# Kernel optimization log

Hardware: AMD Instinct MI355X
Metric: run time of the kernel (lower is better)

## Reference

```python
import jax, jax.numpy as jnp
import numpy as np
from jax import lax


def leaky(x):
    return jax.nn.leaky_relu(x, 0.01)


def masked_softmax(vec, mask, eps=1e-6):
    # softmax over entries where mask>0; zero elsewhere (stable via masked max)
    mask = mask.astype(vec.dtype)
    mx = jnp.max(jnp.where(mask > 0, vec, -jnp.inf), axis=1, keepdims=True)
    mx = jnp.where(jnp.isfinite(mx), mx, 0.0)
    e = jnp.exp(vec - mx) * mask
    return e / (e.sum(axis=1, keepdims=True) + eps)


def gru_dir(x, w_ih, w_hh, b_ih, b_hh, reverse):
    # PyTorch GRU cell math, one direction. x: [T, in]
    gi_all = x @ w_ih.T + b_ih  # [T, 3*GH], input gates precomputed
    def step(h, gi):
        gh = h @ w_hh.T + b_hh
        i_r, i_z, i_n = jnp.split(gi, 3)
        h_r, h_z, h_n = jnp.split(gh, 3)
        r = jax.nn.sigmoid(i_r + h_r)
        z = jax.nn.sigmoid(i_z + h_z)
        n = jnp.tanh(i_n + r * h_n)
        h2 = (1.0 - z) * n + z * h
        return h2, h2
    h0 = jnp.zeros((w_hh.shape[1],), x.dtype)
    _, ys = lax.scan(step, h0, gi_all, reverse=reverse)
    return ys  # [T, GH]


def setup_inputs():
    key = jax.random.key(0)
    ks = jax.random.split(key, 30)
    W, P, R, H = 128, 4096, 8192, 1024
    GH = H // 2
    s = 0.05
    def nrm(k, shp, sc):
        return jax.random.normal(k, shp, jnp.float32) * sc
    return {
        "word_feat": nrm(ks[0], (W, H), 1.0),
        "phrase_feat": nrm(ks[1], (P, H), 1.0),
        "rel_feat": nrm(ks[2], (R, H), 1.0),
        "w_ih_f": nrm(ks[3], (3 * GH, H), s), "w_hh_f": nrm(ks[4], (3 * GH, GH), s),
        "b_ih_f": nrm(ks[5], (3 * GH,), s), "b_hh_f": nrm(ks[6], (3 * GH,), s),
        "w_ih_b": nrm(ks[7], (3 * GH, H), s), "w_hh_b": nrm(ks[8], (3 * GH, GH), s),
        "b_ih_b": nrm(ks[9], (3 * GH,), s), "b_hh_b": nrm(ks[10], (3 * GH,), s),
        "w2p_w_W": nrm(ks[11], (H, H), s), "w2p_w_b": nrm(ks[12], (H,), s),
        "w2p_p_W": nrm(ks[13], (H, H), s), "w2p_p_b": nrm(ks[14], (H,), s),
        "w2p_t_W": nrm(ks[15], (H, H), s), "w2p_t_b": nrm(ks[16], (H,), s),
        "rel_W": nrm(ks[17], (H, 3 * H), s), "rel_b": nrm(ks[18], (H,), s),
        "att1_W": nrm(ks[19], (H, 4 * H), s), "att1_b": nrm(ks[20], (H,), s),
        "att2_W": nrm(ks[21], (1, H), s), "att2_b": nrm(ks[22], (1,), s),
        "r2p_t_W": nrm(ks[23], (H, H), s), "r2p_t_b": nrm(ks[24], (H,), s),
        "rel_conn_mat": jax.random.randint(ks[25], (2, R), 0, P),
        "word_to_graph_conn": jax.random.randint(ks[26], (P, W), 0, 2),
    }


def reference(word_feat, phrase_feat, rel_feat, w_ih_f, w_hh_f, b_ih_f, b_hh_f,
              w_ih_b, w_hh_b, b_ih_b, b_hh_b, w2p_w_W, w2p_w_b, w2p_p_W, w2p_p_b,
              w2p_t_W, w2p_t_b, rel_W, rel_b, att1_W, att1_b, att2_W, att2_b,
              r2p_t_W, r2p_t_b, rel_conn_mat, word_to_graph_conn):
    H = word_feat.shape[1]
    # bidirectional GRU over the word sequence
    lf = jnp.concatenate([
        gru_dir(word_feat, w_ih_f, w_hh_f, b_ih_f, b_hh_f, False),
        gru_dir(word_feat, w_ih_b, w_hh_b, b_ih_b, b_hh_b, True),
    ], axis=1)  # [T, H]
    ctx = jnp.concatenate([lf[0], lf[-1]])[None, :]  # [1, 2H]
    # word -> phrase attention
    a = (leaky(phrase_feat @ w2p_p_W.T + w2p_p_b)
         @ leaky(word_feat @ w2p_w_W.T + w2p_w_b).T) / jnp.sqrt(jnp.float32(H))
    a = masked_softmax(a, word_to_graph_conn)
    upd = phrase_feat + (a @ word_feat) @ w2p_t_W.T + w2p_t_b  # [P, H]
    # phrase -> rel
    sub, obj = rel_conn_mat[0], rel_conn_mat[1]
    Rn = sub.shape[0]
    Pn = upd.shape[0]
    urel = jnp.concatenate([upd[sub], upd[obj], rel_feat], 1) @ rel_W.T + rel_b  # [R, H]
    # rel -> phrase with sparse connectivity (each rel touches subject+object)
    ar = jnp.arange(Rn)
    mask = jnp.zeros((Pn, Rn), upd.dtype).at[sub, ar].set(1.0).at[obj, ar].set(1.0)
    ix = jnp.concatenate([sub, obj])
    iy = jnp.concatenate([ar, ar])
    fuse = jnp.concatenate(
        [upd[ix], urel[iy], jnp.broadcast_to(ctx, (ix.shape[0], ctx.shape[1]))], 1)  # [2R, 4H]
    s = (leaky(fuse @ att1_W.T + att1_b) @ att2_W.T + att2_b)[:, 0]
    att = jnp.zeros((Pn, Rn), upd.dtype).at[ix, iy].set(s)
    att = masked_softmax(att, mask)
    out_phrase = upd + (att @ urel) @ r2p_t_W.T + r2p_t_b
    return (word_feat, out_phrase, urel)
```

## Files before the change

kernel.cpp:

```cpp
#include <hip/hip_runtime.h>

#define DEV __device__ __forceinline__

typedef short s16x8 __attribute__((ext_vector_type(8)));
typedef float f32x4 __attribute__((ext_vector_type(4)));
typedef __fp16 fp16x8 __attribute__((ext_vector_type(8)));
typedef unsigned short u16;
typedef unsigned long long u64;

constexpr int Wn = 128;
constexpr int Pn = 4096;
constexpr int Rn = 8192;
constexpr int Hn = 1024;

DEV float b2f(u16 u) { union { unsigned i; float f; } x; x.i = (unsigned)u << 16; return x.f; }
DEV u16 f2b(float f) {
  union { float f; unsigned i; } x; x.f = f;
  unsigned r = x.i + 0x7FFF + ((x.i >> 16) & 1);
  return (u16)(r >> 16);
}
DEV u16 f2h(float x) { __fp16 h = (__fp16)x; u16 r; __builtin_memcpy(&r, &h, 2); return r; }
DEV float leaky(float x) { return x >= 0.f ? x : 0.01f * x; }

DEV void load_lds16(const void* g, void* l) {
  __builtin_amdgcn_global_load_lds(
      (const __attribute__((address_space(1))) void*)g,
      (__attribute__((address_space(3))) void*)l, 16, 0, 0);
}

DEV float wred_sum(float v) {
  #pragma unroll
  for (int m = 1; m < 64; m <<= 1) v += __shfl_xor(v, m, 64);
  return v;
}
DEV float wred_max(float v) {
  #pragma unroll
  for (int m = 1; m < 64; m <<= 1) v = fmaxf(v, __shfl_xor(v, m, 64));
  return v;
}

template<bool OUTF32, bool ACT, bool BIAS, bool RES, bool DUAL>
DEV void gemm_tile(char* sm,
    const u16* __restrict__ A, int lda, const u16* __restrict__ B, int ldb,
    void* Cp, int ldc, const float* __restrict__ bias,
    const float* res, int ldr, u16* C16, float alpha, int K, int m0, int n0)
{
  char* As = sm;
  char* Bs = sm + 16384;
  const int tid = threadIdx.x;
  const int lane = tid & 63, w = tid >> 6;
  const int wr = (w >> 1) * 64, wc = (w & 1) * 64;
  const int r_lo = lane & 15, kq = lane >> 4;

  __syncthreads();

  f32x4 acc[4][4];
  #pragma unroll
  for (int i = 0; i < 4; ++i)
    #pragma unroll
    for (int j = 0; j < 4; ++j) acc[i][j] = (f32x4){0.f, 0.f, 0.f, 0.f};

  for (int kt = 0; kt < K; kt += 64) {
    if (kt) __syncthreads();
    #pragma unroll
    for (int i = 0; i < 4; ++i) {
      int f = i * 4096 + tid * 16;
      int row = f >> 7, colb = f & 127;
      int scol = colb ^ ((row & 7) << 4);
      load_lds16((const char*)(A + (size_t)(m0 + row) * lda + kt) + scol,
                 As + i * 4096 + w * 1024);
    }
    #pragma unroll
    for (int i = 0; i < 4; ++i) {
      int f = i * 4096 + tid * 16;
      int row = f >> 7, colb = f & 127;
      int scol = colb ^ ((row & 7) << 4);
      load_lds16((const char*)(B + (size_t)(n0 + row) * ldb + kt) + scol,
                 Bs + i * 4096 + w * 1024);
    }
    __syncthreads();
    #pragma unroll
    for (int ks = 0; ks < 2; ++ks) {
      s16x8 af[4], bfr[4];
      const int kb = ks * 64 + kq * 16;
      #pragma unroll
      for (int mi = 0; mi < 4; ++mi) {
        int row = wr + mi * 16 + r_lo;
        af[mi] = *(const s16x8*)(As + row * 128 + (kb ^ ((row & 7) << 4)));
      }
      #pragma unroll
      for (int ni = 0; ni < 4; ++ni) {
        int row = wc + ni * 16 + r_lo;
        bfr[ni] = *(const s16x8*)(Bs + row * 128 + (kb ^ ((row & 7) << 4)));
      }
      #pragma unroll
      for (int mi = 0; mi < 4; ++mi)
        #pragma unroll
        for (int ni = 0; ni < 4; ++ni)
          acc[mi][ni] = __builtin_amdgcn_mfma_f32_16x16x32_bf16(af[mi], bfr[ni], acc[mi][ni], 0, 0, 0);
    }
  }
  #pragma unroll
  for (int mi = 0; mi < 4; ++mi)
    #pragma unroll
    for (int ni = 0; ni < 4; ++ni)
      #pragma unroll
      for (int j = 0; j < 4; ++j) {
        int r = m0 + wr + mi * 16 + kq * 4 + j;
        int c = n0 + wc + ni * 16 + r_lo;
        float v = acc[mi][ni][j] * alpha;
        if (BIAS) v += bias[c];
        if (RES)  v += res[(size_t)r * ldr + c];
        if (ACT)  v = leaky(v);
        if (OUTF32) ((float*)Cp)[(size_t)r * ldc + c] = v;
        else        ((u16*)Cp)[(size_t)r * ldc + c] = f2b(v);
        if (DUAL)   C16[(size_t)r * ldc + c] = f2b(v);
      }
}

template<bool OUTF32, bool ACT, bool BIAS, bool RES, bool DUAL>
__global__ __launch_bounds__(256) void k_gemm_bt(
    const u16* __restrict__ A, int lda, const u16* __restrict__ B, int ldb,
    void* Cp, int ldc, const float* __restrict__ bias,
    const float* res, int ldr, u16* C16, float alpha, int K)
{
  __shared__ __align__(16) char sm[32768];
  gemm_tile<OUTF32, ACT, BIAS, RES, DUAL>(sm, A, lda, B, ldb, Cp, ldc, bias,
      res, ldr, C16, alpha, K, blockIdx.y * 128, blockIdx.x * 128);
}

DEV void gemm_tile_bf32(char* sm,
    const u16* __restrict__ A, int lda, const float* __restrict__ Bf, int ldb,
    float* __restrict__ C, int ldc, const float* __restrict__ bias,
    int K, int m0, int n0)
{
  char* As = sm;
  char* Bs = sm + 16384;
  const int tid = threadIdx.x;
  const int lane = tid & 63, w = tid >> 6;
  const int wr = (w >> 1) * 64, wc = (w & 1) * 64;
  const int r_lo = lane & 15, kq = lane >> 4;

  __syncthreads();

  f32x4 acc[4][4];
  #pragma unroll
  for (int i = 0; i < 4; ++i)
    #pragma unroll
    for (int j = 0; j < 4; ++j) acc[i][j] = (f32x4){0.f, 0.f, 0.f, 0.f};

  for (int kt = 0; kt < K; kt += 64) {
    if (kt) __syncthreads();
    #pragma unroll
    for (int i = 0; i < 4; ++i) {
      int f = i * 4096 + tid * 16;
      int row = f >> 7, colb = f & 127;
      int scol = colb ^ ((row & 7) << 4);
      load_lds16((const char*)(A + (size_t)(m0 + row) * lda + kt) + scol,
                 As + i * 4096 + w * 1024);
    }
    #pragma unroll
    for (int i = 0; i < 4; ++i) {
      int e = i * 2048 + tid * 8;
      int row = e >> 6, col = e & 63;
      const float* s = Bf + (size_t)(n0 + row) * ldb + kt + col;
      float4 a4 = *(const float4*)s;
      float4 b4 = *(const float4*)(s + 4);
      u16 d8[8] = {f2b(a4.x), f2b(a4.y), f2b(a4.z), f2b(a4.w),
                   f2b(b4.x), f2b(b4.y), f2b(b4.z), f2b(b4.w)};
      int byte = (col * 2) ^ ((row & 7) << 4);
      *(uint4*)(Bs + row * 128 + byte) = *(uint4*)d8;
    }
    __syncthreads();
    #pragma unroll
    for (int ks = 0; ks < 2; ++ks) {
      s16x8 af[4], bfr[4];
      const int kb = ks * 64 + kq * 16;
      #pragma unroll
      for (int mi = 0; mi < 4; ++mi) {
        int row = wr + mi * 16 + r_lo;
        af[mi] = *(const s16x8*)(As + row * 128 + (kb ^ ((row & 7) << 4)));
      }
      #pragma unroll
      for (int ni = 0; ni < 4; ++ni) {
        int row = wc + ni * 16 + r_lo;
        bfr[ni] = *(const s16x8*)(Bs + row * 128 + (kb ^ ((row & 7) << 4)));
      }
      #pragma unroll
      for (int mi = 0; mi < 4; ++mi)
        #pragma unroll
        for (int ni = 0; ni < 4; ++ni)
          acc[mi][ni] = __builtin_amdgcn_mfma_f32_16x16x32_bf16(af[mi], bfr[ni], acc[mi][ni], 0, 0, 0);
    }
  }
  #pragma unroll
  for (int mi = 0; mi < 4; ++mi)
    #pragma unroll
    for (int ni = 0; ni < 4; ++ni)
      #pragma unroll
      for (int j = 0; j < 4; ++j) {
        int r = m0 + wr + mi * 16 + kq * 4 + j;
        int c = n0 + wc + ni * 16 + r_lo;
        C[(size_t)r * ldc + c] = acc[mi][ni][j] + bias[c];
      }
}

__global__ __launch_bounds__(256) void k_gemm_af32(
    const float* __restrict__ A, int lda, const u16* __restrict__ B, int ldb,
    u16* __restrict__ C, int ldc, int K)
{
  __shared__ __align__(16) char sm[32768];
  char* As = sm;
  char* Bs = sm + 16384;
  const int tid = threadIdx.x;
  const int lane = tid & 63, w = tid >> 6;
  const int m0 = blockIdx.y * 128, n0 = blockIdx.x * 128;
  const int wr = (w >> 1) * 64, wc = (w & 1) * 64;
  const int r_lo = lane & 15, kq = lane >> 4;

  f32x4 acc[4][4];
  #pragma unroll
  for (int i = 0; i < 4; ++i)
    #pragma unroll
    for (int j = 0; j < 4; ++j) acc[i][j] = (f32x4){0.f, 0.f, 0.f, 0.f};

  for (int kt = 0; kt < K; kt += 64) {
    if (kt) __syncthreads();
    #pragma unroll
    for (int i = 0; i < 4; ++i) {
      int e = i * 2048 + tid * 8;
      int row = e >> 6, col = e & 63;
      const float* s = A + (size_t)(m0 + row) * lda + kt + col;
      float4 a4 = *(const float4*)s;
      float4 b4 = *(const float4*)(s + 4);
      u16 d8[8] = {f2b(a4.x), f2b(a4.y), f2b(a4.z), f2b(a4.w),
                   f2b(b4.x), f2b(b4.y), f2b(b4.z), f2b(b4.w)};
      int byte = (col * 2) ^ ((row & 7) << 4);
      *(uint4*)(As + row * 128 + byte) = *(uint4*)d8;
    }
    #pragma unroll
    for (int i = 0; i < 4; ++i) {
      int f = i * 4096 + tid * 16;
      int row = f >> 7, colb = f & 127;
      int scol = colb ^ ((row & 7) << 4);
      load_lds16((const char*)(B + (size_t)(n0 + row) * ldb + kt) + scol,
                 Bs + i * 4096 + w * 1024);
    }
    __syncthreads();
    #pragma unroll
    for (int ks = 0; ks < 2; ++ks) {
      s16x8 af[4], bfr[4];
      const int kb = ks * 64 + kq * 16;
      #pragma unroll
      for (int mi = 0; mi < 4; ++mi) {
        int row = wr + mi * 16 + r_lo;
        af[mi] = *(const s16x8*)(As + row * 128 + (kb ^ ((row & 7) << 4)));
      }
      #pragma unroll
      for (int ni = 0; ni < 4; ++ni) {
        int row = wc + ni * 16 + r_lo;
        bfr[ni] = *(const s16x8*)(Bs + row * 128 + (kb ^ ((row & 7) << 4)));
      }
      #pragma unroll
      for (int mi = 0; mi < 4; ++mi)
        #pragma unroll
        for (int ni = 0; ni < 4; ++ni)
          acc[mi][ni] = __builtin_amdgcn_mfma_f32_16x16x32_bf16(af[mi], bfr[ni], acc[mi][ni], 0, 0, 0);
    }
  }
  #pragma unroll
  for (int mi = 0; mi < 4; ++mi)
    #pragma unroll
    for (int ni = 0; ni < 4; ++ni)
      #pragma unroll
      for (int j = 0; j < 4; ++j) {
        int r = m0 + wr + mi * 16 + kq * 4 + j;
        int c = n0 + wc + ni * 16 + r_lo;
        C[(size_t)r * ldc + c] = f2b(acc[mi][ni][j]);
      }
}

__global__ __launch_bounds__(256) void k_rf3(
    const u16* __restrict__ G, const u16* __restrict__ relU,
    const u16* __restrict__ W3s, const float* __restrict__ rel_b,
    float* __restrict__ out_urel)
{
  __shared__ __align__(16) char sm[32768];
  int half = blockIdx.y >> 5;
  gemm_tile<true, false, true, false, false>(sm,
      half ? relU : G, Hn, W3s, Hn,
      out_urel + (size_t)half * 4096 * Hn, Hn, rel_b, nullptr, 0, nullptr,
      1.f, Hn, (blockIdx.y & 31) * 128, blockIdx.x * 128);
}

__global__ __launch_bounds__(256) void k_gemm_rel(
    const u16* __restrict__ upd16, const int* __restrict__ rcm,
    const u16* __restrict__ W1, const u16* __restrict__ W2,
    float* __restrict__ out_urel)
{
  __shared__ __align__(16) char sm[32768];
  __shared__ int ridx[2][128];
  char* As = sm;
  char* Bs = sm + 16384;
  const int tid = threadIdx.x;
  const int lane = tid & 63, w = tid >> 6;
  const int hh = blockIdx.y >> 5;
  const int m0 = (blockIdx.y & 31) * 128, n0 = blockIdx.x * 128;
  const int wr = (w >> 1) * 64, wc = (w & 1) * 64;
  const int r_lo = lane & 15, kq = lane >> 4;
  const int* sub = rcm + hh * 4096;
  const int* obj = rcm + Rn + hh * 4096;
  float* C = out_urel + (size_t)hh * 4096 * Hn;

  if (tid < 128) ridx[0][tid] = sub[m0 + tid];
  else ridx[1][tid - 128] = obj[m0 + tid - 128];
  __syncthreads();

  f32x4 acc[4][4];
  #pragma unroll
  for (int i = 0; i < 4; ++i)
    #pragma unroll
    for (int j = 0; j < 4; ++j) acc[i][j] = (f32x4){0.f, 0.f, 0.f, 0.f};

  for (int kt = 0; kt < 2048; kt += 64) {
    const int half = kt >> 10;
    const int kk = kt & 1023;
    const u16* Wm = half ? W2 : W1;
    __syncthreads();
    #pragma unroll
    for (int i = 0; i < 4; ++i) {
      int f = i * 4096 + tid * 16;
      int row = f >> 7, colb = f & 127;
      int scol = colb ^ ((row & 7) << 4);
      load_lds16((const char*)(upd16 + (size_t)ridx[half][row] * 1024 + kk) + scol,
                 As + i * 4096 + w * 1024);
    }
    #pragma unroll
    for (int i = 0; i < 4; ++i) {
      int f = i * 4096 + tid * 16;
      int row = f >> 7, colb = f & 127;
      int scol = colb ^ ((row & 7) << 4);
      load_lds16((const char*)(Wm + (size_t)(n0 + row) * 1024 + kk) + scol,
                 Bs + i * 4096 + w * 1024);
    }
    __syncthreads();
    #pragma unroll
    for (int ks = 0; ks < 2; ++ks) {
      s16x8 af[4], bfr[4];
      const int kb = ks * 64 + kq * 16;
      #pragma unroll
      for (int mi = 0; mi < 4; ++mi) {
        int row = wr + mi * 16 + r_lo;
        af[mi] = *(const s16x8*)(As + row * 128 + (kb ^ ((row & 7) << 4)));
      }
      #pragma unroll
      for (int ni = 0; ni < 4; ++ni) {
        int row = wc + ni * 16 + r_lo;
        bfr[ni] = *(const s16x8*)(Bs + row * 128 + (kb ^ ((row & 7) << 4)));
      }
      #pragma unroll
      for (int mi = 0; mi < 4; ++mi)
        #pragma unroll
        for (int ni = 0; ni < 4; ++ni)
          acc[mi][ni] = __builtin_amdgcn_mfma_f32_16x16x32_bf16(af[mi], bfr[ni], acc[mi][ni], 0, 0, 0);
    }
  }
  #pragma unroll
  for (int mi = 0; mi < 4; ++mi)
    #pragma unroll
    for (int ni = 0; ni < 4; ++ni)
      #pragma unroll
      for (int j = 0; j < 4; ++j) {
        int r = m0 + wr + mi * 16 + kq * 4 + j;
        int c = n0 + wc + ni * 16 + r_lo;
        C[(size_t)r * Hn + c] = acc[mi][ni][j] + C[(size_t)r * Hn + c];
      }
}

struct CvtTask { const float* src; u16* dst; int sld; int units; };
struct MKArgs {
  const float *w_hh_f, *w_hh_b, *b_hh_f, *b_hh_b;
  const float *word_feat, *w_ih_f, *w_ih_b, *b_ih_f, *b_ih_b;
  const float *w2p_w_b, *w2p_p_b;
  const int *rcm, *conn;
  float *gi_f, *gi_b, *scores, *ctx;
  u16 *wf16, *wl, *pf16, *w2pw16, *w2pp16, *pl, *attw, *wfT, *aw;
  u64* X; int* pc; int* cnt2; int* offs; int* cursor;
  CvtTask t[12]; int nt;
};

__global__ __launch_bounds__(256) void k_mega(MKArgs a)
{
  __shared__ __align__(16) u16 wlds[96 * 512];
  __shared__ float bh[96];
  __shared__ float partg[4][96];
  __shared__ __align__(16) u16 hb[512];

  const int bid = blockIdx.x;
  const int tid = threadIdx.x;
  const int lane = tid & 63, wv = tid >> 6;
  const int NW = (int)gridDim.x - 32;

  if (bid >= 32) {
    const int bc = bid - 32, nb = NW;
    int bar = 0;
    auto wbarrier = [&]() {
      __syncthreads();
      if (tid == 0) {
        __hip_atomic_fetch_add(&a.pc[bar], 1, __ATOMIC_ACQ_REL, __HIP_MEMORY_SCOPE_AGENT);
        while (__hip_atomic_load(&a.pc[bar], __ATOMIC_ACQUIRE, __HIP_MEMORY_SCOPE_AGENT) < NW)
          __builtin_amdgcn_s_sleep(4);
      }
      __syncthreads();
      ++bar;
    };
    auto cvt_task = [&](const float* src, int sld, u16* dst, int units) {
      for (int u = bc * 256 + tid; u < units; u += nb * 256) {
        int row = u >> 7, c = (u & 127) * 8;
        const float* s = src + (size_t)row * sld + c;
        float4 va = *(const float4*)s;
        float4 vb = *(const float4*)(s + 4);
        ushort4 lo = {f2b(va.x), f2b(va.y), f2b(va.z), f2b(va.w)};
        ushort4 hi = {f2b(vb.x), f2b(vb.y), f2b(vb.z), f2b(vb.w)};
        *(ushort4*)(dst + (size_t)row * 1024 + c) = lo;
        *(ushort4*)(dst + (size_t)row * 1024 + c + 4) = hi;
      }
    };

    cvt_task(a.word_feat, Hn, a.wf16, Wn * 128);
    wbarrier();
    if (bc < 24) {
      const float* Bm = bc < 12 ? a.w_ih_f : a.w_ih_b;
      float* Cm = bc < 12 ? a.gi_f : a.gi_b;
      const float* bm = bc < 12 ? a.b_ih_f : a.b_ih_b;
      gemm_tile_bf32((char*)wlds, a.wf16, Hn, Bm, Hn, Cm, 1536, bm, Hn,
                     0, (bc % 12) * 128);
      __syncthreads();
      if (tid == 0)
        __hip_atomic_fetch_add(&a.pc[32], 1, __ATOMIC_ACQ_REL, __HIP_MEMORY_SCOPE_AGENT);
    }
    for (int u = bc * 256 + tid; u < 2 * Rn; u += nb * 256) {
      if (u < Rn && a.rcm[u] == a.rcm[Rn + u]) continue;
      atomicAdd(a.cnt2 + a.rcm[u], 1);
    }
    for (int k = 0; k < a.nt; ++k)
      cvt_task(a.t[k].src, a.t[k].sld, a.t[k].dst, a.t[k].units);
    wbarrier();
    if (bc == 0) {
      int* part = (int*)wlds;
      int* pscan = part + 256;
      int loc[16]; int s = 0;
      #pragma unroll
      for (int i = 0; i < 16; ++i) { loc[i] = a.cnt2[tid * 16 + i]; s += loc[i]; }
      part[tid] = s; __syncthreads();
      if (tid == 0) { int acc = 0; for (int i = 0; i < 256; ++i) { pscan[i] = acc; acc += part[i]; } }
      __syncthreads();
      int base = pscan[tid];
      #pragma unroll
      for (int i = 0; i < 16; ++i) {
        a.offs[tid * 16 + i] = base; a.cursor[tid * 16 + i] = base; base += loc[i];
      }
      if (tid == 255) a.offs[Pn] = base;
      __syncthreads();
    }
    for (int u = bc; u < 264; u += nb) {
      if (u < 8)
        gemm_tile<false, true, true, false, false>((char*)wlds, a.wf16, Hn,
            a.w2pw16, Hn, a.wl, Hn, a.w2p_w_b, nullptr, 0, nullptr, 1.f, Hn,
            0, u * 128);
      else {
        int t2 = u - 8;
        gemm_tile<false, true, true, false, false>((char*)wlds, a.pf16, Hn,
            a.w2pp16, Hn, a.pl, Hn, a.w2p_p_b, nullptr, 0, nullptr, 1.f, Hn,
            (t2 >> 3) * 128, (t2 & 7) * 128);
      }
    }
    wbarrier();
    for (int u = bc; u < 544; u += nb) {
      if (u < 32)
        gemm_tile<true, false, false, false, false>((char*)wlds, a.pl, Hn,
            a.wl, Hn, a.scores, Wn, nullptr, nullptr, 0, nullptr, 0.03125f, Hn,
            u * 128, 0);
      else {
        int idx = (u - 32) * 256 + tid;
        int r = idx >> 10, c = idx & 1023;
        a.wfT[c * 128 + r] = a.wf16[idx];
      }
    }
    wbarrier();
    for (int u = bc; u < 1024; u += nb) {
      int p = u * 4 + wv;
      float v0 = a.scores[(size_t)p * 128 + lane];
      float v1 = a.scores[(size_t)p * 128 + 64 + lane];
      int m0 = a.conn[(size_t)p * 128 + lane];
      int m1 = a.conn[(size_t)p * 128 + 64 + lane];
      float x0 = m0 > 0 ? v0 : -INFINITY;
      float x1 = m1 > 0 ? v1 : -INFINITY;
      float mx = wred_max(fmaxf(x0, x1));
      if (!(mx > -INFINITY)) mx = 0.f;
      float e0 = m0 > 0 ? __expf(v0 - mx) : 0.f;
      float e1 = m1 > 0 ? __expf(v1 - mx) : 0.f;
      float s = wred_sum(e0 + e1);
      float inv = 1.f / (s + 1e-6f);
      a.attw[(size_t)p * 128 + lane] = f2b(e0 * inv);
      a.attw[(size_t)p * 128 + 64 + lane] = f2b(e1 * inv);
    }
    wbarrier();
    for (int u = bc; u < 256; u += nb)
      gemm_tile<false, false, false, false, false>((char*)wlds, a.attw, Wn,
          a.wfT, Wn, a.aw, Hn, nullptr, nullptr, 0, nullptr, 1.f, Wn,
          (u >> 3) * 128, (u & 7) * 128);
    return;
  }

  const int dir = bid >> 4;
  const int b   = bid & 15;
  const float* w_hh = dir ? a.w_hh_b : a.w_hh_f;
  const float* b_hhp = dir ? a.b_hh_b : a.b_hh_f;
  const float* gi = dir ? a.gi_b : a.gi_f;
  u64* Xd = a.X + (size_t)dir * 128 * 256;

  for (int idx = tid; idx < 96 * 128; idx += 256) {
    int gl = idx >> 7;
    int kc = (idx & 127) << 2;
    int g  = 32 * b + (gl & 31) + ((gl >> 5) << 9);
    float4 wv4 = *(const float4*)(w_hh + (size_t)g * 512 + kc);
    u16 d4[4] = {f2h(wv4.x), f2h(wv4.y), f2h(wv4.z), f2h(wv4.w)};
    int byte = (kc * 2) ^ ((gl & 7) << 4);
    *(uint2*)((char*)wlds + gl * 1024 + byte) = *(uint2*)d4;
  }
  if (tid < 96) {
    int g = 32 * b + (tid & 31) + ((tid >> 5) << 9);
    bh[tid] = b_hhp[g];
  }
  for (int i = tid; i < 256; i += 256) ((unsigned*)hb)[i] = 0u;
  if (tid == 0) {
    while (__hip_atomic_load(&a.pc[32], __ATOMIC_ACQUIRE, __HIP_MEMORY_SCOPE_AGENT) < 24)
      __builtin_amdgcn_s_sleep(8);
  }
  __syncthreads();

  float hprev = 0.f;
  const int jg = 32 * b + tid;
  const int r_lo = lane & 15, kq = lane >> 4;
  const fp16x8 zf = {0, 0, 0, 0, 0, 0, 0, 0};

  for (int sidx = 0; sidx < 128; ++sidx) {
    const int t = dir ? (127 - sidx) : sidx;

    float gir = 0.f, giz = 0.f, gin = 0.f;
    if (tid < 32) {
      gir = gi[t * 1536 + jg];
      giz = gi[t * 1536 + 512 + jg];
      gin = gi[t * 1536 + 1024 + jg];
    }

    f32x4 acc6[6];
    #pragma unroll
    for (int gt = 0; gt < 6; ++gt) acc6[gt] = (f32x4){0.f, 0.f, 0.f, 0.f};
    #pragma unroll
    for (int k2 = 0; k2 < 4; ++k2) {
      int kt = (wv << 2) + k2;
      fp16x8 bf = (r_lo == 0) ? *(const fp16x8*)(hb + kt * 32 + kq * 8) : zf;
      #pragma unroll
      for (int gt = 0; gt < 6; ++gt) {
        int gl = gt * 16 + r_lo;
        int byte = (kt * 64 + kq * 16) ^ ((gl & 7) << 4);
        fp16x8 af = *(const fp16x8*)((const char*)wlds + gl * 1024 + byte);
        acc6[gt] = __builtin_amdgcn_mfma_f32_16x16x32_f16(af, bf, acc6[gt], 0, 0, 0);
      }
    }
    if (r_lo == 0) {
      #pragma unroll
      for (int gt = 0; gt < 6; ++gt)
        #pragma unroll
        for (int j = 0; j < 4; ++j)
          partg[wv][gt * 16 + kq * 4 + j] = acc6[gt][j];
    }
    __syncthreads();

    if (wv == 0) {
      float h2v = 0.f;
      if (lane < 32) {
        int j = lane;
        float ghr = partg[0][j] + partg[1][j] + partg[2][j] + partg[3][j] + bh[j];
        float ghz = partg[0][j + 32] + partg[1][j + 32] + partg[2][j + 32] + partg[3][j + 32] + bh[j + 32];
        float ghn = partg[0][j + 64] + partg[1][j + 64] + partg[2][j + 64] + partg[3][j + 64] + bh[j + 64];
        float rr = 1.f / (1.f + __expf(-(gir + ghr)));
        float zz = 1.f / (1.f + __expf(-(giz + ghz)));
        float nn = tanhf(gin + rr * ghn);
        h2v = (1.f - zz) * nn + zz * hprev;
        hprev = h2v;
        if (sidx == 0)   a.ctx[(dir ? 1536 : 0)    + jg] = h2v;
        if (sidx == 127) a.ctx[(dir ? 512  : 1024) + jg] = h2v;
      }
      if (sidx < 127) {
        float q0 = __shfl(h2v, (lane & 15) * 2, 64);
        float q1 = __shfl(h2v, (lane & 15) * 2 + 1, 64);
        if (lane < 16) {
          u64 pk = (u64)f2h(q0) | ((u64)f2h(q1) << 16) |
                   ((u64)(unsigned)(sidx + 1) << 32);
          __hip_atomic_store(&Xd[(size_t)sidx * 256 + b * 16 + lane], pk,
                             __ATOMIC_RELAXED, __HIP_MEMORY_SCOPE_AGENT);
        }
        const u64* src = Xd + (size_t)sidx * 256;
        const unsigned want = (unsigned)(sidx + 1);
        const int base = lane * 4;
        u64 v[4];
        unsigned done = 0;
        while (done != 0xFu) {
          #pragma unroll
          for (int i = 0; i < 4; ++i)
            if (!(done & (1u << i)))
              v[i] = __hip_atomic_load(&src[base + i], __ATOMIC_RELAXED,
                                       __HIP_MEMORY_SCOPE_AGENT);
          #pragma unroll
          for (int i = 0; i < 4; ++i)
            if (!(done & (1u << i)) && (unsigned)(v[i] >> 32) == want)
              done |= 1u << i;
          if (done != 0xFu) __builtin_amdgcn_s_sleep(1);
        }
        #pragma unroll
        for (int i = 0; i < 4; ++i)
          ((unsigned*)hb)[base + i] = (unsigned)v[i];
      }
    }
    __syncthreads();
  }
}

__global__ __launch_bounds__(256) void k_cvec(const float* __restrict__ att1W,
    const float* __restrict__ att1b, const float* __restrict__ ctx, float* __restrict__ cvec)
{
  int i = blockIdx.x * 4 + (threadIdx.x >> 6);
  int lane = threadIdx.x & 63;
  const float* wrow = att1W + (size_t)i * 4096 + 2048 + lane * 32;
  const float* cp = ctx + lane * 32;
  float acc = 0.f;
  #pragma unroll
  for (int k = 0; k < 32; ++k) acc += wrow[k] * cp[k];
  acc = wred_sum(acc);
  if (lane == 0) cvec[i] = acc + att1b[i];
}

__global__ __launch_bounds__(256) void k_edge_s(const int* __restrict__ rcm,
    const u16* __restrict__ U1, const u16* __restrict__ V1, const float* __restrict__ cvec,
    const float* __restrict__ att2w, const float* __restrict__ att2b,
    float* __restrict__ sval)
{
  int idx = blockIdx.x * 4 + (threadIdx.x >> 6);
  int lane = threadIdx.x & 63;
  int rL = idx < Rn ? idx : idx - Rn;
  int p = rcm[idx];
  const u16* u = U1 + (size_t)p * Hn + lane * 16;
  const u16* v = V1 + (size_t)rL * Hn + lane * 16;
  const float* aw = att2w + lane * 16;
  const float* cv = cvec + lane * 16;
  float acc = 0.f;
  #pragma unroll
  for (int i = 0; i < 16; ++i) {
    float x = b2f(u[i]) + b2f(v[i]) + cv[i];
    acc += aw[i] * leaky(x);
  }
  acc = wred_sum(acc);
  if (lane == 0) sval[idx] = acc + att2b[0];
}

__global__ __launch_bounds__(256) void k_fill(const int* __restrict__ rcm,
    const float* __restrict__ sval, int* __restrict__ cursor,
    int* __restrict__ er, float* __restrict__ es)
{
  int e = blockIdx.x * 256 + threadIdx.x;
  if (e < Rn && rcm[e] == rcm[Rn + e]) return;
  int slot = atomicAdd(cursor + rcm[e], 1);
  er[slot] = e & (Rn - 1);
  es[slot] = sval[e];
}

__global__ __launch_bounds__(256) void k_att_apply(const int* __restrict__ offs,
    const int* __restrict__ er, const float* __restrict__ es,
    const float* __restrict__ urel, u16* __restrict__ pacc)
{
  int p = blockIdx.x;
  int tid = threadIdx.x;
  int beg = offs[p], end = offs[p + 1];
  float mx = -INFINITY;
  for (int i = beg; i < end; ++i) mx = fmaxf(mx, es[i]);
  float den = 1e-6f;
  for (int i = beg; i < end; ++i) den += __expf(es[i] - mx);
  float inv = 1.f / den;
  float a0 = 0.f, a1 = 0.f, a2 = 0.f, a3 = 0.f;
  int c0 = tid * 4;
  for (int i = beg; i < end; ++i) {
    float wgt = __expf(es[i] - mx) * inv;
    float4 q = *(const float4*)(urel + (size_t)er[i] * Hn + c0);
    a0 += wgt * q.x; a1 += wgt * q.y; a2 += wgt * q.z; a3 += wgt * q.w;
  }
  ushort4 ov; ov.x = f2b(a0); ov.y = f2b(a1); ov.z = f2b(a2); ov.w = f2b(a3);
  *(ushort4*)(pacc + (size_t)p * Hn + c0) = ov;
}

extern "C" void kernel_launch(void* const* d_in, const int* in_sizes, int n_in,
                              void* d_out, int out_size, void* d_ws, size_t ws_size,
                              hipStream_t stream)
{
  const float* word_feat   = (const float*)d_in[0];
  const float* phrase_feat = (const float*)d_in[1];
  const float* rel_feat    = (const float*)d_in[2];
  const float* w_ih_f = (const float*)d_in[3];
  const float* w_hh_f = (const float*)d_in[4];
  const float* b_ih_f = (const float*)d_in[5];
  const float* b_hh_f = (const float*)d_in[6];
  const float* w_ih_b = (const float*)d_in[7];
  const float* w_hh_b = (const float*)d_in[8];
  const float* b_ih_b = (const float*)d_in[9];
  const float* b_hh_b = (const float*)d_in[10];
  const float* w2p_w_W = (const float*)d_in[11];
  const float* w2p_w_b = (const float*)d_in[12];
  const float* w2p_p_W = (const float*)d_in[13];
  const float* w2p_p_b = (const float*)d_in[14];
  const float* w2p_t_W = (const float*)d_in[15];
  const float* w2p_t_b = (const float*)d_in[16];
  const float* rel_W   = (const float*)d_in[17];
  const float* rel_b   = (const float*)d_in[18];
  const float* att1_W  = (const float*)d_in[19];
  const float* att1_b  = (const float*)d_in[20];
  const float* att2_W  = (const float*)d_in[21];
  const float* att2_b  = (const float*)d_in[22];
  const float* r2p_t_W = (const float*)d_in[23];
  const float* r2p_t_b = (const float*)d_in[24];
  const int* rcm  = (const int*)d_in[25];
  const int* conn = (const int*)d_in[26];

  float* out_word = (float*)d_out;
  float* out_phr  = out_word + (size_t)Wn * Hn;
  float* out_urel = out_phr + (size_t)Pn * Hn;

  char* ws = (char*)d_ws;
  size_t off = 0;
  auto alloc = [&](size_t bytes) -> char* {
    char* pptr = ws + off; off += (bytes + 255) & ~(size_t)255; return pptr;
  };
  int*   cnt2   = (int*)alloc(Pn * 4);
  int*   pc     = (int*)alloc(64 * 4);
  u64*   X      = (u64*)alloc(2 * 128 * 256 * 8);
  size_t zlen   = (size_t)((char*)(X + 2 * 128 * 256) - (char*)cnt2);
  float* ctx    = (float*)alloc(2048 * 4);
  float* cvec   = (float*)alloc(1024 * 4);
  int*   cursor = (int*)alloc(Pn * 4);
  int*   offs   = (int*)alloc((Pn + 1) * 4);
  int*   er     = (int*)alloc(2 * Rn * 4);
  float* es     = (float*)alloc(2 * Rn * 4);
  float* sval   = (float*)alloc(2 * Rn * 4);
  float* gi_f   = (float*)alloc(128 * 1536 * 4);
  float* gi_b   = (float*)alloc(128 * 1536 * 4);
  u16*   wf16   = (u16*)alloc((size_t)Wn * Hn * 2);
  u16*   wl     = (u16*)alloc((size_t)Wn * Hn * 2);
  u16*   upd16  = (u16*)alloc((size_t)Pn * Hn * 2);
  char*  RA     = alloc(16777216);
  u16*   W1s    = (u16*)RA;
  u16*   W2s    = (u16*)(RA + 2097152);
  u16*   W3s    = (u16*)(RA + 4194304);
  u16*   G      = (u16*)(RA + 6291456);
  u16*   V1f    = (u16*)RA;
  u16*   A1p16  = (u16*)alloc(2097152);
  u16*   A1r16  = (u16*)alloc(2097152);
  u16*   U1     = (u16*)alloc((size_t)Pn * Hn * 2);
  u16*   relU16 = U1;
  u16*   r2pW16 = (u16*)alloc(2097152);
  u16*   pacc   = upd16;

  float* scores = (float*)out_phr;
  char* urlB = (char*)out_urel;
  u16*   pf16   = (u16*)urlB;
  u16*   w2pw16 = (u16*)(urlB + 8388608);
  u16*   w2pp16 = (u16*)(urlB + 10485760);
  u16*   w2pt16 = (u16*)(urlB + 12582912);
  u16*   pl     = (u16*)(urlB + 14680064);
  u16*   aw     = (u16*)(urlB + 23068672);
  u16*   attw   = (u16*)(urlB + 31457280);
  u16*   wfT    = (u16*)(urlB + 32505856);

  (void)hipMemsetAsync(cnt2, 0, zlen, stream);

  dim3 blk(256);

  MKArgs A;
  A.w_hh_f = w_hh_f; A.w_hh_b = w_hh_b; A.b_hh_f = b_hh_f; A.b_hh_b = b_hh_b;
  A.word_feat = word_feat; A.w_ih_f = w_ih_f; A.w_ih_b = w_ih_b;
  A.b_ih_f = b_ih_f; A.b_ih_b = b_ih_b;
  A.w2p_w_b = w2p_w_b; A.w2p_p_b = w2p_p_b;
  A.rcm = rcm; A.conn = conn;
  A.gi_f = gi_f; A.gi_b = gi_b; A.scores = scores; A.ctx = ctx;
  A.wf16 = wf16; A.wl = wl;
  A.pf16 = pf16; A.w2pw16 = w2pw16; A.w2pp16 = w2pp16;
  A.pl = pl; A.attw = attw; A.wfT = wfT; A.aw = aw;
  A.X = X; A.pc = pc; A.cnt2 = cnt2; A.offs = offs; A.cursor = cursor;
  A.t[0]  = {phrase_feat,    pf16,   Hn,     Pn * 128};
  A.t[1]  = {w2p_w_W,        w2pw16, Hn,     1024 * 128};
  A.t[2]  = {w2p_p_W,        w2pp16, Hn,     1024 * 128};
  A.t[3]  = {w2p_t_W,        w2pt16, Hn,     1024 * 128};
  A.t[4]  = {rel_W,          W1s,    3 * Hn, 1024 * 128};
  A.t[5]  = {rel_W + Hn,     W2s,    3 * Hn, 1024 * 128};
  A.t[6]  = {rel_W + 2 * Hn, W3s,    3 * Hn, 1024 * 128};
  A.t[7]  = {att1_W,         A1p16,  4 * Hn, 1024 * 128};
  A.t[8]  = {att1_W + Hn,    A1r16,  4 * Hn, 1024 * 128};
  A.t[9]  = {r2p_t_W,        r2pW16, Hn,     1024 * 128};
  A.t[10] = {rel_feat,       G,      Hn,     4096 * 128};
  A.t[11] = {rel_feat + (size_t)4096 * Hn, relU16, Hn, 4096 * 128};
  A.nt = 12;
  k_mega<<<256, blk, 0, stream>>>(A);
  k_cvec<<<256, blk, 0, stream>>>(att1_W, att1_b, ctx, cvec);

  k_gemm_bt<true, false, true, true, true><<<dim3(8, 32), blk, 0, stream>>>(
      aw, Hn, w2pt16, Hn, out_phr, Hn, w2p_t_b, phrase_feat, Hn, upd16, 1.f, Hn);

  k_rf3<<<dim3(8, 64), blk, 0, stream>>>(G, relU16, W3s, rel_b, out_urel);
  k_gemm_rel<<<dim3(8, 64), blk, 0, stream>>>(upd16, rcm, W1s, W2s, out_urel);

  k_gemm_bt<false, false, false, false, false><<<dim3(8, 32), blk, 0, stream>>>(
      upd16, Hn, A1p16, Hn, U1, Hn, nullptr, nullptr, 0, nullptr, 1.f, Hn);
  k_gemm_af32<<<dim3(8, 64), blk, 0, stream>>>(
      out_urel, Hn, A1r16, Hn, V1f, Hn, Hn);

  k_edge_s<<<(2 * Rn) / 4, blk, 0, stream>>>(rcm, U1, V1f, cvec, att2_W, att2_b, sval);
  k_fill<<<(2 * Rn) / 256, blk, 0, stream>>>(rcm, sval, cursor, er, es);
  k_att_apply<<<Pn, blk, 0, stream>>>(offs, er, es, out_urel, pacc);
  k_gemm_bt<true, false, true, true, false><<<dim3(8, 32), blk, 0, stream>>>(
      pacc, Hn, r2pW16, Hn, out_phr, Hn, r2p_t_b, out_phr, Hn, nullptr, 1.f, Hn);

  (void)hipMemcpyAsync(out_word, word_feat, (size_t)Wn * Hn * 4,
                       hipMemcpyDeviceToDevice, stream);
}
```

Before: 764.6 us.

## Hold GRU recurrent weights in registers, widen persistent mega-kernel, fuse w2p_t GEMM

The GRU blocks now keep their W_hh fp16 MFMA fragments in registers instead of a 96KB LDS tile. That lets shared memory shrink to 32KB and allows three blocks per CU under launch_bounds(256,3). The grid grows from 256 to 736 blocks, giving the worker phase many more blocks. The separate w2p_t GEMM launch is folded into the mega-kernel after an extra grid barrier. This raises register pressure and relies on all 736 blocks being co-resident for the spin barriers, so it risks spills or deadlock if occupancy falls short.

```diff
diff --git a/kernel.cpp b/kernel.cpp
--- a/kernel.cpp
+++ b/kernel.cpp
@@ -381,17 +381,17 @@
 struct MKArgs {
   const float *w_hh_f, *w_hh_b, *b_hh_f, *b_hh_b;
   const float *word_feat, *w_ih_f, *w_ih_b, *b_ih_f, *b_ih_b;
-  const float *w2p_w_b, *w2p_p_b;
+  const float *phrase_feat, *w2p_w_b, *w2p_p_b, *w2p_t_b;
   const int *rcm, *conn;
-  float *gi_f, *gi_b, *scores, *ctx;
-  u16 *wf16, *wl, *pf16, *w2pw16, *w2pp16, *pl, *attw, *wfT, *aw;
+  float *gi_f, *gi_b, *scores, *out_phr, *ctx;
+  u16 *wf16, *wl, *pf16, *w2pw16, *w2pp16, *w2pt16, *pl, *attw, *wfT, *aw, *upd16;
   u64* X; int* pc; int* cnt2; int* offs; int* cursor;
   CvtTask t[12]; int nt;
 };
 
-__global__ __launch_bounds__(256) void k_mega(MKArgs a)
-{
-  __shared__ __align__(16) u16 wlds[96 * 512];
+__global__ __launch_bounds__(256, 3) void k_mega(MKArgs a)
+{
+  __shared__ __align__(16) char sm[32768];
   __shared__ float bh[96];
   __shared__ float partg[4][96];
   __shared__ __align__(16) u16 hb[512];
@@ -433,7 +433,7 @@
       const float* Bm = bc < 12 ? a.w_ih_f : a.w_ih_b;
       float* Cm = bc < 12 ? a.gi_f : a.gi_b;
       const float* bm = bc < 12 ? a.b_ih_f : a.b_ih_b;
-      gemm_tile_bf32((char*)wlds, a.wf16, Hn, Bm, Hn, Cm, 1536, bm, Hn,
+      gemm_tile_bf32(sm, a.wf16, Hn, Bm, Hn, Cm, 1536, bm, Hn,
                      0, (bc % 12) * 128);
       __syncthreads();
       if (tid == 0)
@@ -447,7 +447,7 @@
       cvt_task(a.t[k].src, a.t[k].sld, a.t[k].dst, a.t[k].units);
     wbarrier();
     if (bc == 0) {
-      int* part = (int*)wlds;
+      int* part = (int*)sm;
       int* pscan = part + 256;
       int loc[16]; int s = 0;
       #pragma unroll
@@ -465,12 +465,12 @@
     }
     for (int u = bc; u < 264; u += nb) {
       if (u < 8)
-        gemm_tile<false, true, true, false, false>((char*)wlds, a.wf16, Hn,
+        gemm_tile<false, true, true, false, false>(sm, a.wf16, Hn,
             a.w2pw16, Hn, a.wl, Hn, a.w2p_w_b, nullptr, 0, nullptr, 1.f, Hn,
             0, u * 128);
       else {
         int t2 = u - 8;
-        gemm_tile<false, true, true, false, false>((char*)wlds, a.pf16, Hn,
+        gemm_tile<false, true, true, false, false>(sm, a.pf16, Hn,
             a.w2pp16, Hn, a.pl, Hn, a.w2p_p_b, nullptr, 0, nullptr, 1.f, Hn,
             (t2 >> 3) * 128, (t2 & 7) * 128);
       }
@@ -478,7 +478,7 @@
     wbarrier();
     for (int u = bc; u < 544; u += nb) {
       if (u < 32)
-        gemm_tile<true, false, false, false, false>((char*)wlds, a.pl, Hn,
+        gemm_tile<true, false, false, false, false>(sm, a.pl, Hn,
             a.wl, Hn, a.scores, Wn, nullptr, nullptr, 0, nullptr, 0.03125f, Hn,
             u * 128, 0);
       else {
@@ -507,9 +507,14 @@
     }
     wbarrier();
     for (int u = bc; u < 256; u += nb)
-      gemm_tile<false, false, false, false, false>((char*)wlds, a.attw, Wn,
+      gemm_tile<false, false, false, false, false>(sm, a.attw, Wn,
           a.wfT, Wn, a.aw, Hn, nullptr, nullptr, 0, nullptr, 1.f, Wn,
           (u >> 3) * 128, (u & 7) * 128);
+    wbarrier();
+    for (int u = bc; u < 256; u += nb)
+      gemm_tile<true, false, true, true, true>(sm, a.aw, Hn,
+          a.w2pt16, Hn, a.out_phr, Hn, a.w2p_t_b, a.phrase_feat, Hn, a.upd16,
+          1.f, Hn, (u >> 3) * 128, (u & 7) * 128);
     return;
   }
 
@@ -519,15 +524,27 @@
   const float* b_hhp = dir ? a.b_hh_b : a.b_hh_f;
   const float* gi = dir ? a.gi_b : a.gi_f;
   u64* Xd = a.X + (size_t)dir * 128 * 256;
-
-  for (int idx = tid; idx < 96 * 128; idx += 256) {
-    int gl = idx >> 7;
-    int kc = (idx & 127) << 2;
-    int g  = 32 * b + (gl & 31) + ((gl >> 5) << 9);
-    float4 wv4 = *(const float4*)(w_hh + (size_t)g * 512 + kc);
-    u16 d4[4] = {f2h(wv4.x), f2h(wv4.y), f2h(wv4.z), f2h(wv4.w)};
-    int byte = (kc * 2) ^ ((gl & 7) << 4);
-    *(uint2*)((char*)wlds + gl * 1024 + byte) = *(uint2*)d4;
+  const int r_lo = lane & 15, kq = lane >> 4;
+
+  fp16x8 wfrag[4][6];
+  #pragma unroll
+  for (int k2 = 0; k2 < 4; ++k2) {
+    int kt = (wv << 2) + k2;
+    int col = kt * 32 + kq * 8;
+    #pragma unroll
+    for (int gt = 0; gt < 6; ++gt) {
+      int gl = gt * 16 + r_lo;
+      int g = 32 * b + (gl & 31) + ((gl >> 5) << 9);
+      const float* s = w_hh + (size_t)g * 512 + col;
+      float4 lo4 = *(const float4*)s;
+      float4 hi4 = *(const float4*)(s + 4);
+      fp16x8 f;
+      f[0] = (__fp16)lo4.x; f[1] = (__fp16)lo4.y;
+      f[2] = (__fp16)lo4.z; f[3] = (__fp16)lo4.w;
+      f[4] = (__fp16)hi4.x; f[5] = (__fp16)hi4.y;
+      f[6] = (__fp16)hi4.z; f[7] = (__fp16)hi4.w;
+      wfrag[k2][gt] = f;
+    }
   }
   if (tid < 96) {
     int g = 32 * b + (tid & 31) + ((tid >> 5) << 9);
@@ -542,7 +559,6 @@
 
   float hprev = 0.f;
   const int jg = 32 * b + tid;
-  const int r_lo = lane & 15, kq = lane >> 4;
   const fp16x8 zf = {0, 0, 0, 0, 0, 0, 0, 0};
 
   for (int sidx = 0; sidx < 128; ++sidx) {
@@ -563,12 +579,8 @@
       int kt = (wv << 2) + k2;
       fp16x8 bf = (r_lo == 0) ? *(const fp16x8*)(hb + kt * 32 + kq * 8) : zf;
       #pragma unroll
-      for (int gt = 0; gt < 6; ++gt) {
-        int gl = gt * 16 + r_lo;
-        int byte = (kt * 64 + kq * 16) ^ ((gl & 7) << 4);
-        fp16x8 af = *(const fp16x8*)((const char*)wlds + gl * 1024 + byte);
-        acc6[gt] = __builtin_amdgcn_mfma_f32_16x16x32_f16(af, bf, acc6[gt], 0, 0, 0);
-      }
+      for (int gt = 0; gt < 6; ++gt)
+        acc6[gt] = __builtin_amdgcn_mfma_f32_16x16x32_f16(wfrag[k2][gt], bf, acc6[gt], 0, 0, 0);
     }
     if (r_lo == 0) {
       #pragma unroll
@@ -789,12 +801,12 @@
   A.w_hh_f = w_hh_f; A.w_hh_b = w_hh_b; A.b_hh_f = b_hh_f; A.b_hh_b = b_hh_b;
   A.word_feat = word_feat; A.w_ih_f = w_ih_f; A.w_ih_b = w_ih_b;
   A.b_ih_f = b_ih_f; A.b_ih_b = b_ih_b;
-  A.w2p_w_b = w2p_w_b; A.w2p_p_b = w2p_p_b;
-  A.rcm = rcm; A.conn = conn;
-  A.gi_f = gi_f; A.gi_b = gi_b; A.scores = scores; A.ctx = ctx;
+  A.phrase_feat = phrase_feat; A.w2p_w_b = w2p_w_b; A.w2p_p_b = w2p_p_b;
+  A.w2p_t_b = w2p_t_b; A.rcm = rcm; A.conn = conn;
+  A.gi_f = gi_f; A.gi_b = gi_b; A.scores = scores; A.out_phr = out_phr; A.ctx = ctx;
   A.wf16 = wf16; A.wl = wl;
-  A.pf16 = pf16; A.w2pw16 = w2pw16; A.w2pp16 = w2pp16;
-  A.pl = pl; A.attw = attw; A.wfT = wfT; A.aw = aw;
+  A.pf16 = pf16; A.w2pw16 = w2pw16; A.w2pp16 = w2pp16; A.w2pt16 = w2pt16;
+  A.pl = pl; A.attw = attw; A.wfT = wfT; A.aw = aw; A.upd16 = upd16;
   A.X = X; A.pc = pc; A.cnt2 = cnt2; A.offs = offs; A.cursor = cursor;
   A.t[0]  = {phrase_feat,    pf16,   Hn,     Pn * 128};
   A.t[1]  = {w2p_w_W,        w2pw16, Hn,     1024 * 128};
@@ -809,11 +821,8 @@
   A.t[10] = {rel_feat,       G,      Hn,     4096 * 128};
   A.t[11] = {rel_feat + (size_t)4096 * Hn, relU16, Hn, 4096 * 128};
   A.nt = 12;
-  k_mega<<<256, blk, 0, stream>>>(A);
+  k_mega<<<736, blk, 0, stream>>>(A);
   k_cvec<<<256, blk, 0, stream>>>(att1_W, att1_b, ctx, cvec);
-
-  k_gemm_bt<true, false, true, true, true><<<dim3(8, 32), blk, 0, stream>>>(
-      aw, Hn, w2pt16, Hn, out_phr, Hn, w2p_t_b, phrase_feat, Hn, upd16, 1.f, Hn);
 
   k_rf3<<<dim3(8, 64), blk, 0, stream>>>(G, relU16, W3s, rel_b, out_urel);
   k_gemm_rel<<<dim3(8, 64), blk, 0, stream>>>(upd16, rcm, W1s, W2s, out_urel);
```

Result: slower. 1.437 ms (+88.0%).
